# Optimization experiments

Hardware: AMD Instinct MI355X
Metric: run time of the kernel (lower is better)

Reference implementation:

```python
import jax, jax.numpy as jnp
import numpy as np

MAX_LENGTH = 13
PAD_TOKEN = 0
HIDDEN = 1024
VOCAB = 32000
BATCH = 64


def gru_cell(x, h, w_ih, w_hh, b_ih, b_hh):
    # PyTorch GRU gate order: reset, update, new
    gi = x @ w_ih.T + b_ih            # [B, 3H]
    gh = h @ w_hh.T + b_hh            # [B, 3H]
    i_r, i_z, i_n = jnp.split(gi, 3, axis=-1)
    h_r, h_z, h_n = jnp.split(gh, 3, axis=-1)
    r = jax.nn.sigmoid(i_r + h_r)
    z = jax.nn.sigmoid(i_z + h_z)
    n = jnp.tanh(i_n + r * h_n)
    return (1.0 - z) * n + z * h


def setup_inputs() -> dict:
    key = jax.random.key(0)
    ks = jax.random.split(key, 9)
    s = 0.02
    return {
        "encoder_outputs": jax.random.normal(ks[0], (BATCH, MAX_LENGTH, HIDDEN), jnp.float32),
        "encoder_hidden": jax.random.normal(ks[1], (1, BATCH, HIDDEN), jnp.float32),
        "embedding": jax.random.normal(ks[2], (VOCAB, HIDDEN), jnp.float32) * s,
        "w_ih": jax.random.normal(ks[3], (3 * HIDDEN, HIDDEN), jnp.float32) * s,
        "w_hh": jax.random.normal(ks[4], (3 * HIDDEN, HIDDEN), jnp.float32) * s,
        "b_ih": jnp.zeros((3 * HIDDEN,), jnp.float32),
        "b_hh": jnp.zeros((3 * HIDDEN,), jnp.float32),
        "w_out": jax.random.normal(ks[5], (VOCAB, HIDDEN), jnp.float32) * s,
        "b_out": jnp.zeros((VOCAB,), jnp.float32),
    }


def reference(encoder_outputs, encoder_hidden, embedding, w_ih, w_hh, b_ih, b_hh, w_out, b_out):
    batch = encoder_outputs.shape[0]
    h0 = encoder_hidden[0]                               # [B, H]
    tok0 = jnp.full((batch,), PAD_TOKEN, dtype=jnp.int32)

    def step(carry, _):
        h, tok = carry
        x = jax.nn.relu(embedding[tok])                  # embed + relu
        h = gru_cell(x, h, w_ih, w_hh, b_ih, b_hh)       # GRU cell
        logits = h @ w_out.T + b_out                     # [B, V]
        nxt = jnp.argmax(logits, axis=-1).astype(jnp.int32)  # greedy feedback (topk(1))
        return (h, nxt), logits

    (h_final, _), logits = jax.lax.scan(step, (h0, tok0), None, length=MAX_LENGTH)
    logits = jnp.transpose(logits, (1, 0, 2))            # [B, T, V]
    log_probs = jax.nn.log_softmax(logits, axis=-1)
    return log_probs, h_final[None]
```

## Files before the change

kernel.cpp:

```cpp
#include <hip/hip_runtime.h>
#include <math.h>

#define BB 64
#define HH 1024
#define VV 32000
#define TT 13
#define QS 8000
#define BKL 128

typedef float f32x4 __attribute__((ext_vector_type(4)));
typedef __bf16 bf16x8 __attribute__((ext_vector_type(8)));

__device__ __forceinline__ unsigned short f2bf(float f) {
  unsigned u = __float_as_uint(f);
  u = (u + 0x7fffu + ((u >> 16) & 1u)) >> 16;
  return (unsigned short)u;
}
__device__ __forceinline__ float bf2f(unsigned short s) {
  return __uint_as_float(((unsigned)s) << 16);
}

__device__ __forceinline__ void gld16(const void* g, void* l) {
  __builtin_amdgcn_global_load_lds(
      (const __attribute__((address_space(1))) unsigned int*)g,
      (__attribute__((address_space(3))) unsigned int*)l, 16, 0, 0);
}

__global__ __launch_bounds__(1024) void k_init(
    const float* __restrict__ enc, const float* __restrict__ emb,
    float* __restrict__ hrm, unsigned short* __restrict__ hhi,
    unsigned short* __restrict__ hlo, unsigned short* __restrict__ xhi,
    unsigned short* __restrict__ xlo) {
  const int g = blockIdx.x * 1024 + threadIdx.x;
  const float h = enc[g];
  hrm[g] = h;
  const unsigned short h16 = f2bf(h);
  hhi[g] = h16;
  hlo[g] = f2bf(h - bf2f(h16));
  float e = emb[threadIdx.x];
  e = e > 0.f ? e : 0.f;
  const unsigned short e16 = f2bf(e);
  xhi[g] = e16;
  xlo[g] = f2bf(e - bf2f(e16));
}

__global__ __launch_bounds__(256) void k_wconv(const float* __restrict__ w,
                                               unsigned short* __restrict__ o) {
  const int n4 = VV * HH / 4;
  for (int i = blockIdx.x * 256 + threadIdx.x; i < n4; i += gridDim.x * 256) {
    const f32x4 v = ((const f32x4*)w)[i];
    ushort4 u;
    u.x = f2bf(v[0]); u.y = f2bf(v[1]); u.z = f2bf(v[2]); u.w = f2bf(v[3]);
    ((ushort4*)o)[i] = u;
  }
}

__global__ __launch_bounds__(256) void k_wconv2(
    const float* __restrict__ wih, const float* __restrict__ whh,
    unsigned short* __restrict__ ghi, unsigned short* __restrict__ glo) {
  const int n4 = 6 * HH * HH / 4;
  for (int i = blockIdx.x * 256 + threadIdx.x; i < n4; i += gridDim.x * 256) {
    const int flat = i * 4;
    const float* src = flat < 3 * HH * HH ? wih + flat : whh + (flat - 3 * HH * HH);
    const f32x4 v = *(const f32x4*)src;
    ushort4 hi, lo;
    hi.x = f2bf(v[0]); lo.x = f2bf(v[0] - bf2f(hi.x));
    hi.y = f2bf(v[1]); lo.y = f2bf(v[1] - bf2f(hi.y));
    hi.z = f2bf(v[2]); lo.z = f2bf(v[2] - bf2f(hi.z));
    hi.w = f2bf(v[3]); lo.w = f2bf(v[3] - bf2f(hi.w));
    ((ushort4*)ghi)[i] = hi;
    ((ushort4*)glo)[i] = lo;
  }
}

__global__ __launch_bounds__(64) void k_gru(
    const unsigned short* __restrict__ xhi, const unsigned short* __restrict__ xlo,
    const unsigned short* __restrict__ hhi_s, const unsigned short* __restrict__ hlo_s,
    const unsigned short* __restrict__ ghi, const unsigned short* __restrict__ glo,
    const float* __restrict__ wih, const float* __restrict__ whh,
    float* __restrict__ gbuf, int cachegw) {
  const int blk = blockIdx.x, lane = threadIdx.x;
  const int kh = blk & 1;
  const int r2 = blk >> 1;
  const int g6 = r2 % 6, jt = r2 / 6;
  const unsigned short* Ahi = g6 < 3 ? xhi : hhi_s;
  const unsigned short* Alo = g6 < 3 ? xlo : hlo_s;
  const int cl = lane & 15, kk = (lane >> 4) * 8;
  const int j = jt * 16 + cl;
  const int kbeg = kh * 512;
  f32x4 acc[4];
  acc[0] = acc[1] = acc[2] = acc[3] = (f32x4){0.f, 0.f, 0.f, 0.f};

  if (cachegw) {
    const unsigned short* bh = ghi + (size_t)(g6 * HH + j) * HH + kbeg;
    const unsigned short* bl = glo + (size_t)(g6 * HH + j) * HH + kbeg;
    const unsigned short* ah = Ahi + kbeg;
    const unsigned short* al = Alo + kbeg;
    #pragma unroll 4
    for (int k0 = 0; k0 < 512; k0 += 32) {
      const bf16x8 whi = *(const bf16x8*)(bh + k0 + kk);
      const bf16x8 wlo = *(const bf16x8*)(bl + k0 + kk);
      #pragma unroll
      for (int rt = 0; rt < 4; ++rt) {
        const size_t aoff = (size_t)(rt * 16 + cl) * HH + k0 + kk;
        const bf16x8 a_h = *(const bf16x8*)(ah + aoff);
        const bf16x8 a_l = *(const bf16x8*)(al + aoff);
        acc[rt] = __builtin_amdgcn_mfma_f32_16x16x32_bf16(a_h, whi, acc[rt], 0, 0, 0);
        acc[rt] = __builtin_amdgcn_mfma_f32_16x16x32_bf16(a_l, whi, acc[rt], 0, 0, 0);
        acc[rt] = __builtin_amdgcn_mfma_f32_16x16x32_bf16(a_h, wlo, acc[rt], 0, 0, 0);
      }
    }
  } else {
    const float* W = (g6 < 3 ? wih : whh) + (size_t)((g6 % 3) * HH + j) * HH + kbeg;
    for (int k0 = 0; k0 < 512; k0 += 32) {
      const f32x4 w0 = *(const f32x4*)(W + k0 + kk);
      const f32x4 w1 = *(const f32x4*)(W + k0 + kk + 4);
      union { unsigned short u[8]; bf16x8 b; } chi, clo;
      #pragma unroll
      for (int u2 = 0; u2 < 4; ++u2) {
        chi.u[u2] = f2bf(w0[u2]); clo.u[u2] = f2bf(w0[u2] - bf2f(chi.u[u2]));
        chi.u[4 + u2] = f2bf(w1[u2]); clo.u[4 + u2] = f2bf(w1[u2] - bf2f(chi.u[4 + u2]));
      }
      #pragma unroll
      for (int rt = 0; rt < 4; ++rt) {
        const size_t aoff = (size_t)(rt * 16 + cl) * HH + kbeg + k0 + kk;
        const bf16x8 a_h = *(const bf16x8*)(Ahi + aoff);
        const bf16x8 a_l = *(const bf16x8*)(Alo + aoff);
        acc[rt] = __builtin_amdgcn_mfma_f32_16x16x32_bf16(a_h, chi.b, acc[rt], 0, 0, 0);
        acc[rt] = __builtin_amdgcn_mfma_f32_16x16x32_bf16(a_l, chi.b, acc[rt], 0, 0, 0);
        acc[rt] = __builtin_amdgcn_mfma_f32_16x16x32_bf16(a_h, clo.b, acc[rt], 0, 0, 0);
      }
    }
  }
  #pragma unroll
  for (int rt = 0; rt < 4; ++rt)
    #pragma unroll
    for (int rg = 0; rg < 4; ++rg) {
      const int row = rt * 16 + (lane >> 4) * 4 + rg;
      gbuf[(size_t)((kh * 6 + g6) * BB + row) * HH + jt * 16 + cl] = acc[rt][rg];
    }
}

__global__ __launch_bounds__(256) void k_gep(
    const float* __restrict__ gbuf, const float* __restrict__ bih,
    const float* __restrict__ bhh, const float* __restrict__ hsrc,
    float* __restrict__ hdst, unsigned short* __restrict__ hhi_d,
    unsigned short* __restrict__ hlo_d) {
  const int e = blockIdx.x * 256 + threadIdx.x;
  const int b = e >> 10, j = e & (HH - 1);
  const size_t base = (size_t)b * HH + j;
  const float gir = gbuf[(size_t)(0 * BB + b) * HH + j] + gbuf[(size_t)((6 + 0) * BB + b) * HH + j] + bih[j];
  const float giz = gbuf[(size_t)(1 * BB + b) * HH + j] + gbuf[(size_t)((6 + 1) * BB + b) * HH + j] + bih[HH + j];
  const float gin = gbuf[(size_t)(2 * BB + b) * HH + j] + gbuf[(size_t)((6 + 2) * BB + b) * HH + j] + bih[2 * HH + j];
  const float ghr = gbuf[(size_t)(3 * BB + b) * HH + j] + gbuf[(size_t)((6 + 3) * BB + b) * HH + j] + bhh[j];
  const float ghz = gbuf[(size_t)(4 * BB + b) * HH + j] + gbuf[(size_t)((6 + 4) * BB + b) * HH + j] + bhh[HH + j];
  const float ghn = gbuf[(size_t)(5 * BB + b) * HH + j] + gbuf[(size_t)((6 + 5) * BB + b) * HH + j] + bhh[2 * HH + j];
  const float r_ = 1.f / (1.f + __expf(-(gir + ghr)));
  const float z_ = 1.f / (1.f + __expf(-(giz + ghz)));
  const float n_ = tanhf(gin + r_ * ghn);
  const float hnew = (1.f - z_) * n_ + z_ * hsrc[base];
  hdst[base] = hnew;
  const unsigned short h16 = f2bf(hnew);
  hhi_d[base] = h16;
  hlo_d[base] = f2bf(hnew - bf2f(h16));
}

__global__ __launch_bounds__(512, 1) void k_logits_lds(
    const unsigned short* __restrict__ hb,
    const unsigned short* __restrict__ wbf,
    const float* __restrict__ bout, float* __restrict__ lbuf) {
  __shared__ __attribute__((aligned(16))) unsigned char sA[2][64 * BKL * 2];
  __shared__ __attribute__((aligned(16))) unsigned char sB[2][128 * BKL * 2];
  const int tid = threadIdx.x, blk = blockIdx.x;
  const int lane = tid & 63, wv = tid >> 6;
  const int cl = lane & 15, kk = (lane >> 4) * 8;

  auto STAGE = [&](int buf, int k0) {
    #pragma unroll
    for (int it = 0; it < 2; ++it) {
      const int c = it * 512 + tid;
      const int r = c >> 4;
      const int kb = (c & 15) * 16;
      const int kbs = kb ^ ((r & 7) << 4);
      gld16(hb + (size_t)r * HH + k0 + (kbs >> 1),
            &sA[buf][it * 8192 + wv * 1024]);
    }
    #pragma unroll
    for (int it = 0; it < 4; ++it) {
      const int c = it * 512 + tid;
      const int col = c >> 4;
      const int kb = (c & 15) * 16;
      const int kbs = kb ^ ((col & 7) << 4);
      gld16(wbf + (size_t)(blk * 128 + col) * HH + k0 + (kbs >> 1),
            &sB[buf][it * 8192 + wv * 1024]);
    }
  };

  f32x4 acc[4];
  acc[0] = acc[1] = acc[2] = acc[3] = (f32x4){0.f, 0.f, 0.f, 0.f};

  STAGE(0, 0);
  for (int t = 0; t < HH / BKL; ++t) {
    const int cur = t & 1;
    if (t < HH / BKL - 1) {
      STAGE(cur ^ 1, (t + 1) * BKL);
      asm volatile("s_waitcnt vmcnt(6)" ::: "memory");
    } else {
      asm volatile("s_waitcnt vmcnt(0)" ::: "memory");
    }
    __builtin_amdgcn_s_barrier();
    __builtin_amdgcn_sched_barrier(0);
    #pragma unroll
    for (int ks = 0; ks < BKL; ks += 32) {
      const int bc = wv * 16 + cl;
      const bf16x8 bfr = *(const bf16x8*)&sB[cur][bc * (BKL * 2) + (((ks + kk) * 2) ^ ((bc & 7) << 4))];
      #pragma unroll
      for (int rt = 0; rt < 4; ++rt) {
        const int ar = rt * 16 + cl;
        const bf16x8 afr = *(const bf16x8*)&sA[cur][ar * (BKL * 2) + (((ks + kk) * 2) ^ ((ar & 7) << 4))];
        acc[rt] = __builtin_amdgcn_mfma_f32_16x16x32_bf16(afr, bfr, acc[rt], 0, 0, 0);
      }
    }
    __builtin_amdgcn_s_barrier();
    __builtin_amdgcn_sched_barrier(0);
  }

  const int col = blk * 128 + wv * 16 + cl;
  const float bo = bout[col];
  #pragma unroll
  for (int rt = 0; rt < 4; ++rt)
    #pragma unroll
    for (int rg = 0; rg < 4; ++rg) {
      const int row = rt * 16 + (lane >> 4) * 4 + rg;
      lbuf[(size_t)row * VV + col] = acc[rt][rg] + bo;
    }
}

__global__ __launch_bounds__(256) void k_logits_fb(
    const unsigned short* __restrict__ hb, const float* __restrict__ wout,
    const float* __restrict__ bout, float* __restrict__ lbuf) {
  const int tid = threadIdx.x, blk = blockIdx.x;
  const int lane = tid & 63, wv = tid >> 6;
  const int n0 = blk * 64 + wv * 16;
  const int cl = lane & 15, kk = (lane >> 4) * 8;
  f32x4 acc[4];
  acc[0] = acc[1] = acc[2] = acc[3] = (f32x4){0.f, 0.f, 0.f, 0.f};
  const float* wrow = wout + (size_t)(n0 + cl) * HH;
  for (int k0 = 0; k0 < HH; k0 += 32) {
    const f32x4 w0 = *(const f32x4*)(wrow + k0 + kk);
    const f32x4 w1 = *(const f32x4*)(wrow + k0 + kk + 4);
    union { unsigned short u[8]; bf16x8 b; } cv;
    #pragma unroll
    for (int u2 = 0; u2 < 4; ++u2) { cv.u[u2] = f2bf(w0[u2]); cv.u[4 + u2] = f2bf(w1[u2]); }
    #pragma unroll
    for (int rt = 0; rt < 4; ++rt) {
      const bf16x8 afr = *(const bf16x8*)(hb + (size_t)(rt * 16 + cl) * HH + k0 + kk);
      acc[rt] = __builtin_amdgcn_mfma_f32_16x16x32_bf16(afr, cv.b, acc[rt], 0, 0, 0);
    }
  }
  const int col = n0 + cl;
  const float bo = bout[col];
  #pragma unroll
  for (int rt = 0; rt < 4; ++rt)
    #pragma unroll
    for (int rg = 0; rg < 4; ++rg) {
      const int row = rt * 16 + (lane >> 4) * 4 + rg;
      lbuf[(size_t)row * VV + col] = acc[rt][rg] + bo;
    }
}

__global__ __launch_bounds__(256) void k_sum(
    const float* __restrict__ lbuf, const float* __restrict__ wout,
    const float* __restrict__ bout, const float* __restrict__ hnew,
    float* __restrict__ mq, float* __restrict__ sq,
    float* __restrict__ qbestV, int* __restrict__ qbestI, int dorecheck) {
  __shared__ float srow[QS];
  __shared__ float red[4];
  __shared__ int icnt;
  __shared__ int scand[32];
  const int tid = threadIdx.x;
  const int b = blockIdx.x >> 2, q = blockIdx.x & 3;
  const int lane = tid & 63, wv = tid >> 6;
  const f32x4* src = (const f32x4*)(lbuf + (size_t)b * VV + q * QS);
  f32x4* s4 = (f32x4*)srow;

  float m = -3.0e38f;
  for (int i = tid; i < QS / 4; i += 256) {
    const f32x4 v = src[i];
    s4[i] = v;
    m = fmaxf(fmaxf(fmaxf(m, v[0]), v[1]), fmaxf(v[2], v[3]));
  }
  #pragma unroll
  for (int d = 1; d < 64; d <<= 1) m = fmaxf(m, __shfl_xor(m, d, 64));
  if (lane == 0) red[wv] = m;
  if (tid == 0) icnt = 0;
  __syncthreads();
  const float M = fmaxf(fmaxf(red[0], red[1]), fmaxf(red[2], red[3]));

  float s = 0.f;
  for (int i = tid; i < QS / 4; i += 256) {
    const f32x4 v = s4[i];
    s += __expf(v[0] - M) + __expf(v[1] - M) + __expf(v[2] - M) + __expf(v[3] - M);
  }
  #pragma unroll
  for (int d = 1; d < 64; d <<= 1) s += __shfl_xor(s, d, 64);
  __syncthreads();
  if (lane == 0) red[wv] = s;
  __syncthreads();
  if (tid == 0) {
    mq[b * 4 + q] = M;
    sq[b * 4 + q] = red[0] + red[1] + red[2] + red[3];
  }

  if (dorecheck) {
    const float thr = M - 0.05f;
    for (int i = tid; i < QS / 4; i += 256) {
      const f32x4 v = s4[i];
      #pragma unroll
      for (int u = 0; u < 4; ++u)
        if (v[u] >= thr) {
          const int c = atomicAdd(&icnt, 1);
          if (c < 32) scand[c] = q * QS + 4 * i + u;
        }
    }
    __syncthreads();
    if (wv == 0) {
      const int nc = icnt < 32 ? icnt : 32;
      const float* hrow = hnew + (size_t)b * HH;
      f32x4 h4[4];
      #pragma unroll
      for (int u = 0; u < 4; ++u) h4[u] = *(const f32x4*)(hrow + lane * 16 + u * 4);
      float best = -3.0e38f; int bi = 0x7fffffff;
      for (int ci = 0; ci < nc; ++ci) {
        const int v = scand[ci];
        const float* wrow = wout + (size_t)v * HH + lane * 16;
        float ss = 0.f;
        #pragma unroll
        for (int u = 0; u < 4; ++u) {
          const f32x4 w4 = *(const f32x4*)(wrow + u * 4);
          ss += h4[u][0] * w4[0] + h4[u][1] * w4[1] + h4[u][2] * w4[2] + h4[u][3] * w4[3];
        }
        #pragma unroll
        for (int d = 1; d < 64; d <<= 1) ss += __shfl_xor(ss, d, 64);
        ss += bout[v];
        if (ss > best || (ss == best && v < bi)) { best = ss; bi = v; }
      }
      if (lane == 0) { qbestV[b * 4 + q] = best; qbestI[b * 4 + q] = bi; }
    }
  }
}

__global__ __launch_bounds__(256) void k_out(
    const float* __restrict__ lbuf, const float* __restrict__ mq,
    const float* __restrict__ sq, const float* __restrict__ qbestV,
    const int* __restrict__ qbestI, const float* __restrict__ emb,
    const float* __restrict__ hnew, float* __restrict__ out,
    unsigned short* __restrict__ xhi, unsigned short* __restrict__ xlo, int t) {
  __shared__ int stok;
  const int tid = threadIdx.x;
  const int b = blockIdx.x >> 2, q = blockIdx.x & 3;

  const float m0 = mq[b * 4 + 0], m1 = mq[b * 4 + 1];
  const float m2 = mq[b * 4 + 2], m3 = mq[b * 4 + 3];
  const float Mg = fmaxf(fmaxf(m0, m1), fmaxf(m2, m3));
  const float Sg = sq[b * 4 + 0] * __expf(m0 - Mg) + sq[b * 4 + 1] * __expf(m1 - Mg) +
                   sq[b * 4 + 2] * __expf(m2 - Mg) + sq[b * 4 + 3] * __expf(m3 - Mg);
  const float LZ = Mg + logf(Sg);

  const f32x4* src = (const f32x4*)(lbuf + (size_t)b * VV + q * QS);
  f32x4* dst = (f32x4*)(out + ((size_t)b * TT + t) * VV + q * QS);
  for (int i = tid; i < QS / 4; i += 256)
    dst[i] = src[i] - LZ;

  if (q == 0 && t < TT - 1) {
    if (tid == 0) {
      float bv = qbestV[b * 4 + 0]; int bi = qbestI[b * 4 + 0];
      #pragma unroll
      for (int qq = 1; qq < 4; ++qq) {
        const float v = qbestV[b * 4 + qq]; const int i2 = qbestI[b * 4 + qq];
        if (v > bv || (v == bv && i2 < bi)) { bv = v; bi = i2; }
      }
      stok = bi;
    }
    __syncthreads();
    const int tok = stok;
    for (int j = tid; j < HH; j += 256) {
      float e = emb[(size_t)tok * HH + j];
      e = e > 0.f ? e : 0.f;
      const unsigned short e16 = f2bf(e);
      xhi[(size_t)b * HH + j] = e16;
      xlo[(size_t)b * HH + j] = f2bf(e - bf2f(e16));
    }
  }
  if (q == 0 && t == TT - 1) {
    for (int j = tid; j < HH; j += 256)
      out[(size_t)BB * TT * VV + (size_t)b * HH + j] = hnew[(size_t)b * HH + j];
  }
}

extern "C" void kernel_launch(void* const* d_in, const int* in_sizes, int n_in,
                              void* d_out, int out_size, void* d_ws, size_t ws_size,
                              hipStream_t stream) {
  const float* enc  = (const float*)d_in[1];
  const float* emb  = (const float*)d_in[2];
  const float* wih  = (const float*)d_in[3];
  const float* whh  = (const float*)d_in[4];
  const float* bih  = (const float*)d_in[5];
  const float* bhh  = (const float*)d_in[6];
  const float* wout = (const float*)d_in[7];
  const float* bout = (const float*)d_in[8];
  float* out = (float*)d_out;

  char* ws = (char*)d_ws;
  size_t off = 0;
  auto alloc = [&](size_t bytes) -> char* {
    char* p = ws + off;
    off += (bytes + 255) & ~(size_t)255;
    return p;
  };
  float* hrm = (float*)alloc((size_t)2 * BB * HH * 4);
  unsigned short* hhi = (unsigned short*)alloc((size_t)2 * BB * HH * 2);
  unsigned short* hlo = (unsigned short*)alloc((size_t)2 * BB * HH * 2);
  unsigned short* xhi = (unsigned short*)alloc((size_t)BB * HH * 2);
  unsigned short* xlo = (unsigned short*)alloc((size_t)BB * HH * 2);
  float* gbuf = (float*)alloc((size_t)12 * BB * HH * 4);
  float* lbuf = (float*)alloc((size_t)BB * VV * 4);
  float* mq = (float*)alloc((size_t)BB * 4 * 4);
  float* sq = (float*)alloc((size_t)BB * 4 * 4);
  float* qbestV = (float*)alloc((size_t)BB * 4 * 4);
  int* qbestI = (int*)alloc((size_t)BB * 4 * 4);
  unsigned short* wbf = (unsigned short*)alloc((size_t)VV * HH * 2);
  const int cachew = (ws_size >= off) ? 1 : 0;
  unsigned short* ghi = (unsigned short*)alloc((size_t)6 * HH * HH * 2);
  unsigned short* glo = (unsigned short*)alloc((size_t)6 * HH * HH * 2);
  const int cachegw = (ws_size >= off) ? 1 : 0;

  hipLaunchKernelGGL(k_init, dim3(64), dim3(1024), 0, stream,
                     enc, emb, hrm, hhi, hlo, xhi, xlo);
  if (cachew)
    hipLaunchKernelGGL(k_wconv, dim3(2048), dim3(256), 0, stream, wout, wbf);
  if (cachegw)
    hipLaunchKernelGGL(k_wconv2, dim3(1024), dim3(256), 0, stream, wih, whh, ghi, glo);

  for (int t = 0; t < TT; ++t) {
    const int p = t & 1;
    const float* hsrc = hrm + (size_t)p * BB * HH;
    float* hdst = hrm + (size_t)(p ^ 1) * BB * HH;
    const unsigned short* hhs = hhi + (size_t)p * BB * HH;
    const unsigned short* hls = hlo + (size_t)p * BB * HH;
    unsigned short* hhd = hhi + (size_t)(p ^ 1) * BB * HH;
    unsigned short* hld = hlo + (size_t)(p ^ 1) * BB * HH;

    hipLaunchKernelGGL(k_gru, dim3(768), dim3(64), 0, stream,
                       xhi, xlo, hhs, hls, ghi, glo, wih, whh, gbuf, cachegw);
    hipLaunchKernelGGL(k_gep, dim3(256), dim3(256), 0, stream,
                       gbuf, bih, bhh, hsrc, hdst, hhd, hld);
    if (cachew)
      hipLaunchKernelGGL(k_logits_lds, dim3(250), dim3(512), 0, stream,
                         hhd, wbf, bout, lbuf);
    else
      hipLaunchKernelGGL(k_logits_fb, dim3(500), dim3(256), 0, stream,
                         hhd, wout, bout, lbuf);
    hipLaunchKernelGGL(k_sum, dim3(256), dim3(256), 0, stream,
                       lbuf, wout, bout, hdst, mq, sq, qbestV, qbestI,
                       (t < TT - 1) ? 1 : 0);
    hipLaunchKernelGGL(k_out, dim3(256), dim3(256), 0, stream,
                       lbuf, mq, sq, qbestV, qbestI, emb, hdst, out, xhi, xlo, t);
  }
}
```

Baseline: 927.0 us.

## Fuse GRU gate GEMM and elementwise epilogue into one kernel via LDS

Merges the GRU gate matmul and the gate epilogue into a single kernel. Each of 64 blocks of 12 waves computes all six gate slices and both K-halves for 16 hidden columns, reduces them through shared memory, and writes the new hidden state directly. This removes the global gbuf round trip and one kernel launch per timestep. The trade-off is only 64 workgroups instead of 768, which may underuse the GPU's many CUs during the GEMM phase.

```diff
diff --git a/kernel.cpp b/kernel.cpp
--- a/kernel.cpp
+++ b/kernel.cpp
@@ -73,29 +73,29 @@
   }
 }
 
-__global__ __launch_bounds__(64) void k_gru(
+__global__ __launch_bounds__(768, 1) void k_gruF(
     const unsigned short* __restrict__ xhi, const unsigned short* __restrict__ xlo,
     const unsigned short* __restrict__ hhi_s, const unsigned short* __restrict__ hlo_s,
     const unsigned short* __restrict__ ghi, const unsigned short* __restrict__ glo,
-    const float* __restrict__ wih, const float* __restrict__ whh,
-    float* __restrict__ gbuf, int cachegw) {
-  const int blk = blockIdx.x, lane = threadIdx.x;
-  const int kh = blk & 1;
-  const int r2 = blk >> 1;
-  const int g6 = r2 % 6, jt = r2 / 6;
-  const unsigned short* Ahi = g6 < 3 ? xhi : hhi_s;
-  const unsigned short* Alo = g6 < 3 ? xlo : hlo_s;
+    const float* __restrict__ bih, const float* __restrict__ bhh,
+    const float* __restrict__ hsrc, float* __restrict__ hdst,
+    unsigned short* __restrict__ hhi_d, unsigned short* __restrict__ hlo_d) {
+  __shared__ float g[12][64][17];
+  const int blk = blockIdx.x, tid = threadIdx.x;
+  const int lane = tid & 63, wv = tid >> 6;
+  const int g6 = wv % 6, kh = wv / 6;
   const int cl = lane & 15, kk = (lane >> 4) * 8;
-  const int j = jt * 16 + cl;
+  const int j = blk * 16 + cl;
   const int kbeg = kh * 512;
-  f32x4 acc[4];
-  acc[0] = acc[1] = acc[2] = acc[3] = (f32x4){0.f, 0.f, 0.f, 0.f};
-
-  if (cachegw) {
+  {
+    const unsigned short* Ahi = g6 < 3 ? xhi : hhi_s;
+    const unsigned short* Alo = g6 < 3 ? xlo : hlo_s;
     const unsigned short* bh = ghi + (size_t)(g6 * HH + j) * HH + kbeg;
     const unsigned short* bl = glo + (size_t)(g6 * HH + j) * HH + kbeg;
     const unsigned short* ah = Ahi + kbeg;
     const unsigned short* al = Alo + kbeg;
+    f32x4 acc[4];
+    acc[0] = acc[1] = acc[2] = acc[3] = (f32x4){0.f, 0.f, 0.f, 0.f};
     #pragma unroll 4
     for (int k0 = 0; k0 < 512; k0 += 32) {
       const bf16x8 whi = *(const bf16x8*)(bh + k0 + kk);
@@ -110,59 +110,32 @@
         acc[rt] = __builtin_amdgcn_mfma_f32_16x16x32_bf16(a_h, wlo, acc[rt], 0, 0, 0);
       }
     }
-  } else {
-    const float* W = (g6 < 3 ? wih : whh) + (size_t)((g6 % 3) * HH + j) * HH + kbeg;
-    for (int k0 = 0; k0 < 512; k0 += 32) {
-      const f32x4 w0 = *(const f32x4*)(W + k0 + kk);
-      const f32x4 w1 = *(const f32x4*)(W + k0 + kk + 4);
-      union { unsigned short u[8]; bf16x8 b; } chi, clo;
+    #pragma unroll
+    for (int rt = 0; rt < 4; ++rt)
       #pragma unroll
-      for (int u2 = 0; u2 < 4; ++u2) {
-        chi.u[u2] = f2bf(w0[u2]); clo.u[u2] = f2bf(w0[u2] - bf2f(chi.u[u2]));
-        chi.u[4 + u2] = f2bf(w1[u2]); clo.u[4 + u2] = f2bf(w1[u2] - bf2f(chi.u[4 + u2]));
-      }
-      #pragma unroll
-      for (int rt = 0; rt < 4; ++rt) {
-        const size_t aoff = (size_t)(rt * 16 + cl) * HH + kbeg + k0 + kk;
-        const bf16x8 a_h = *(const bf16x8*)(Ahi + aoff);
-        const bf16x8 a_l = *(const bf16x8*)(Alo + aoff);
-        acc[rt] = __builtin_amdgcn_mfma_f32_16x16x32_bf16(a_h, chi.b, acc[rt], 0, 0, 0);
-        acc[rt] = __builtin_amdgcn_mfma_f32_16x16x32_bf16(a_l, chi.b, acc[rt], 0, 0, 0);
-        acc[rt] = __builtin_amdgcn_mfma_f32_16x16x32_bf16(a_h, clo.b, acc[rt], 0, 0, 0);
-      }
-    }
-  }
-  #pragma unroll
-  for (int rt = 0; rt < 4; ++rt)
-    #pragma unroll
-    for (int rg = 0; rg < 4; ++rg) {
-      const int row = rt * 16 + (lane >> 4) * 4 + rg;
-      gbuf[(size_t)((kh * 6 + g6) * BB + row) * HH + jt * 16 + cl] = acc[rt][rg];
-    }
-}
-
-__global__ __launch_bounds__(256) void k_gep(
-    const float* __restrict__ gbuf, const float* __restrict__ bih,
-    const float* __restrict__ bhh, const float* __restrict__ hsrc,
-    float* __restrict__ hdst, unsigned short* __restrict__ hhi_d,
-    unsigned short* __restrict__ hlo_d) {
-  const int e = blockIdx.x * 256 + threadIdx.x;
-  const int b = e >> 10, j = e & (HH - 1);
-  const size_t base = (size_t)b * HH + j;
-  const float gir = gbuf[(size_t)(0 * BB + b) * HH + j] + gbuf[(size_t)((6 + 0) * BB + b) * HH + j] + bih[j];
-  const float giz = gbuf[(size_t)(1 * BB + b) * HH + j] + gbuf[(size_t)((6 + 1) * BB + b) * HH + j] + bih[HH + j];
-  const float gin = gbuf[(size_t)(2 * BB + b) * HH + j] + gbuf[(size_t)((6 + 2) * BB + b) * HH + j] + bih[2 * HH + j];
-  const float ghr = gbuf[(size_t)(3 * BB + b) * HH + j] + gbuf[(size_t)((6 + 3) * BB + b) * HH + j] + bhh[j];
-  const float ghz = gbuf[(size_t)(4 * BB + b) * HH + j] + gbuf[(size_t)((6 + 4) * BB + b) * HH + j] + bhh[HH + j];
-  const float ghn = gbuf[(size_t)(5 * BB + b) * HH + j] + gbuf[(size_t)((6 + 5) * BB + b) * HH + j] + bhh[2 * HH + j];
-  const float r_ = 1.f / (1.f + __expf(-(gir + ghr)));
-  const float z_ = 1.f / (1.f + __expf(-(giz + ghz)));
-  const float n_ = tanhf(gin + r_ * ghn);
-  const float hnew = (1.f - z_) * n_ + z_ * hsrc[base];
-  hdst[base] = hnew;
-  const unsigned short h16 = f2bf(hnew);
-  hhi_d[base] = h16;
-  hlo_d[base] = f2bf(hnew - bf2f(h16));
+      for (int rg = 0; rg < 4; ++rg)
+        g[wv][rt * 16 + (lane >> 4) * 4 + rg][cl] = acc[rt][rg];
+  }
+  __syncthreads();
+  for (int e = tid; e < BB * 16; e += 768) {
+    const int b = e >> 4, c = e & 15;
+    const int jj = blk * 16 + c;
+    const size_t base = (size_t)b * HH + jj;
+    const float gir = g[0][b][c] + g[6][b][c] + bih[jj];
+    const float giz = g[1][b][c] + g[7][b][c] + bih[HH + jj];
+    const float gin = g[2][b][c] + g[8][b][c] + bih[2 * HH + jj];
+    const float ghr = g[3][b][c] + g[9][b][c] + bhh[jj];
+    const float ghz = g[4][b][c] + g[10][b][c] + bhh[HH + jj];
+    const float ghn = g[5][b][c] + g[11][b][c] + bhh[2 * HH + jj];
+    const float r_ = 1.f / (1.f + __expf(-(gir + ghr)));
+    const float z_ = 1.f / (1.f + __expf(-(giz + ghz)));
+    const float n_ = tanhf(gin + r_ * ghn);
+    const float hnew = (1.f - z_) * n_ + z_ * hsrc[base];
+    hdst[base] = hnew;
+    const unsigned short h16 = f2bf(hnew);
+    hhi_d[base] = h16;
+    hlo_d[base] = f2bf(hnew - bf2f(h16));
+  }
 }
 
 __global__ __launch_bounds__(512, 1) void k_logits_lds(
@@ -226,39 +199,6 @@
   }
 
   const int col = blk * 128 + wv * 16 + cl;
-  const float bo = bout[col];
-  #pragma unroll
-  for (int rt = 0; rt < 4; ++rt)
-    #pragma unroll
-    for (int rg = 0; rg < 4; ++rg) {
-      const int row = rt * 16 + (lane >> 4) * 4 + rg;
-      lbuf[(size_t)row * VV + col] = acc[rt][rg] + bo;
-    }
-}
-
-__global__ __launch_bounds__(256) void k_logits_fb(
-    const unsigned short* __restrict__ hb, const float* __restrict__ wout,
-    const float* __restrict__ bout, float* __restrict__ lbuf) {
-  const int tid = threadIdx.x, blk = blockIdx.x;
-  const int lane = tid & 63, wv = tid >> 6;
-  const int n0 = blk * 64 + wv * 16;
-  const int cl = lane & 15, kk = (lane >> 4) * 8;
-  f32x4 acc[4];
-  acc[0] = acc[1] = acc[2] = acc[3] = (f32x4){0.f, 0.f, 0.f, 0.f};
-  const float* wrow = wout + (size_t)(n0 + cl) * HH;
-  for (int k0 = 0; k0 < HH; k0 += 32) {
-    const f32x4 w0 = *(const f32x4*)(wrow + k0 + kk);
-    const f32x4 w1 = *(const f32x4*)(wrow + k0 + kk + 4);
-    union { unsigned short u[8]; bf16x8 b; } cv;
-    #pragma unroll
-    for (int u2 = 0; u2 < 4; ++u2) { cv.u[u2] = f2bf(w0[u2]); cv.u[4 + u2] = f2bf(w1[u2]); }
-    #pragma unroll
-    for (int rt = 0; rt < 4; ++rt) {
-      const bf16x8 afr = *(const bf16x8*)(hb + (size_t)(rt * 16 + cl) * HH + k0 + kk);
-      acc[rt] = __builtin_amdgcn_mfma_f32_16x16x32_bf16(afr, cv.b, acc[rt], 0, 0, 0);
-    }
-  }
-  const int col = n0 + cl;
   const float bo = bout[col];
   #pragma unroll
   for (int rt = 0; rt < 4; ++rt)
@@ -398,6 +338,108 @@
   }
 }
 
+__global__ __launch_bounds__(64) void k_gru_fb(
+    const unsigned short* __restrict__ xhi, const unsigned short* __restrict__ xlo,
+    const unsigned short* __restrict__ hhi_s, const unsigned short* __restrict__ hlo_s,
+    const float* __restrict__ wih, const float* __restrict__ whh,
+    float* __restrict__ gbuf) {
+  const int blk = blockIdx.x, lane = threadIdx.x;
+  const int kh = blk & 1;
+  const int r2 = blk >> 1;
+  const int g6 = r2 % 6, jt = r2 / 6;
+  const unsigned short* Ahi = g6 < 3 ? xhi : hhi_s;
+  const unsigned short* Alo = g6 < 3 ? xlo : hlo_s;
+  const int cl = lane & 15, kk = (lane >> 4) * 8;
+  const int j = jt * 16 + cl;
+  const int kbeg = kh * 512;
+  f32x4 acc[4];
+  acc[0] = acc[1] = acc[2] = acc[3] = (f32x4){0.f, 0.f, 0.f, 0.f};
+  const float* W = (g6 < 3 ? wih : whh) + (size_t)((g6 % 3) * HH + j) * HH + kbeg;
+  for (int k0 = 0; k0 < 512; k0 += 32) {
+    const f32x4 w0 = *(const f32x4*)(W + k0 + kk);
+    const f32x4 w1 = *(const f32x4*)(W + k0 + kk + 4);
+    union { unsigned short u[8]; bf16x8 b; } chi, clo;
+    #pragma unroll
+    for (int u2 = 0; u2 < 4; ++u2) {
+      chi.u[u2] = f2bf(w0[u2]); clo.u[u2] = f2bf(w0[u2] - bf2f(chi.u[u2]));
+      chi.u[4 + u2] = f2bf(w1[u2]); clo.u[4 + u2] = f2bf(w1[u2] - bf2f(chi.u[4 + u2]));
+    }
+    #pragma unroll
+    for (int rt = 0; rt < 4; ++rt) {
+      const size_t aoff = (size_t)(rt * 16 + cl) * HH + kbeg + k0 + kk;
+      const bf16x8 a_h = *(const bf16x8*)(Ahi + aoff);
+      const bf16x8 a_l = *(const bf16x8*)(Alo + aoff);
+      acc[rt] = __builtin_amdgcn_mfma_f32_16x16x32_bf16(a_h, chi.b, acc[rt], 0, 0, 0);
+      acc[rt] = __builtin_amdgcn_mfma_f32_16x16x32_bf16(a_l, chi.b, acc[rt], 0, 0, 0);
+      acc[rt] = __builtin_amdgcn_mfma_f32_16x16x32_bf16(a_h, clo.b, acc[rt], 0, 0, 0);
+    }
+  }
+  #pragma unroll
+  for (int rt = 0; rt < 4; ++rt)
+    #pragma unroll
+    for (int rg = 0; rg < 4; ++rg) {
+      const int row = rt * 16 + (lane >> 4) * 4 + rg;
+      gbuf[(size_t)((kh * 6 + g6) * BB + row) * HH + jt * 16 + cl] = acc[rt][rg];
+    }
+}
+
+__global__ __launch_bounds__(256) void k_gep(
+    const float* __restrict__ gbuf, const float* __restrict__ bih,
+    const float* __restrict__ bhh, const float* __restrict__ hsrc,
+    float* __restrict__ hdst, unsigned short* __restrict__ hhi_d,
+    unsigned short* __restrict__ hlo_d) {
+  const int e = blockIdx.x * 256 + threadIdx.x;
+  const int b = e >> 10, j = e & (HH - 1);
+  const size_t base = (size_t)b * HH + j;
+  const float gir = gbuf[(size_t)(0 * BB + b) * HH + j] + gbuf[(size_t)((6 + 0) * BB + b) * HH + j] + bih[j];
+  const float giz = gbuf[(size_t)(1 * BB + b) * HH + j] + gbuf[(size_t)((6 + 1) * BB + b) * HH + j] + bih[HH + j];
+  const float gin = gbuf[(size_t)(2 * BB + b) * HH + j] + gbuf[(size_t)((6 + 2) * BB + b) * HH + j] + bih[2 * HH + j];
+  const float ghr = gbuf[(size_t)(3 * BB + b) * HH + j] + gbuf[(size_t)((6 + 3) * BB + b) * HH + j] + bhh[j];
+  const float ghz = gbuf[(size_t)(4 * BB + b) * HH + j] + gbuf[(size_t)((6 + 4) * BB + b) * HH + j] + bhh[HH + j];
+  const float ghn = gbuf[(size_t)(5 * BB + b) * HH + j] + gbuf[(size_t)((6 + 5) * BB + b) * HH + j] + bhh[2 * HH + j];
+  const float r_ = 1.f / (1.f + __expf(-(gir + ghr)));
+  const float z_ = 1.f / (1.f + __expf(-(giz + ghz)));
+  const float n_ = tanhf(gin + r_ * ghn);
+  const float hnew = (1.f - z_) * n_ + z_ * hsrc[base];
+  hdst[base] = hnew;
+  const unsigned short h16 = f2bf(hnew);
+  hhi_d[base] = h16;
+  hlo_d[base] = f2bf(hnew - bf2f(h16));
+}
+
+__global__ __launch_bounds__(256) void k_logits_fb(
+    const unsigned short* __restrict__ hb, const float* __restrict__ wout,
+    const float* __restrict__ bout, float* __restrict__ lbuf) {
+  const int tid = threadIdx.x, blk = blockIdx.x;
+  const int lane = tid & 63, wv = tid >> 6;
+  const int n0 = blk * 64 + wv * 16;
+  const int cl = lane & 15, kk = (lane >> 4) * 8;
+  f32x4 acc[4];
+  acc[0] = acc[1] = acc[2] = acc[3] = (f32x4){0.f, 0.f, 0.f, 0.f};
+  const float* wrow = wout + (size_t)(n0 + cl) * HH;
+  for (int k0 = 0; k0 < HH; k0 += 32) {
+    const f32x4 w0 = *(const f32x4*)(wrow + k0 + kk);
+    const f32x4 w1 = *(const f32x4*)(wrow + k0 + kk + 4);
+    union { unsigned short u[8]; bf16x8 b; } cv;
+    #pragma unroll
+    for (int u2 = 0; u2 < 4; ++u2) { cv.u[u2] = f2bf(w0[u2]); cv.u[4 + u2] = f2bf(w1[u2]); }
+    #pragma unroll
+    for (int rt = 0; rt < 4; ++rt) {
+      const bf16x8 afr = *(const bf16x8*)(hb + (size_t)(rt * 16 + cl) * HH + k0 + kk);
+      acc[rt] = __builtin_amdgcn_mfma_f32_16x16x32_bf16(afr, cv.b, acc[rt], 0, 0, 0);
+    }
+  }
+  const int col = n0 + cl;
+  const float bo = bout[col];
+  #pragma unroll
+  for (int rt = 0; rt < 4; ++rt)
+    #pragma unroll
+    for (int rg = 0; rg < 4; ++rg) {
+      const int row = rt * 16 + (lane >> 4) * 4 + rg;
+      lbuf[(size_t)row * VV + col] = acc[rt][rg] + bo;
+    }
+}
+
 extern "C" void kernel_launch(void* const* d_in, const int* in_sizes, int n_in,
                               void* d_out, int out_size, void* d_ws, size_t ws_size,
                               hipStream_t stream) {
@@ -430,17 +472,16 @@
   float* qbestV = (float*)alloc((size_t)BB * 4 * 4);
   int* qbestI = (int*)alloc((size_t)BB * 4 * 4);
   unsigned short* wbf = (unsigned short*)alloc((size_t)VV * HH * 2);
-  const int cachew = (ws_size >= off) ? 1 : 0;
   unsigned short* ghi = (unsigned short*)alloc((size_t)6 * HH * HH * 2);
   unsigned short* glo = (unsigned short*)alloc((size_t)6 * HH * HH * 2);
-  const int cachegw = (ws_size >= off) ? 1 : 0;
+  const int cache_ok = (ws_size >= off) ? 1 : 0;
 
   hipLaunchKernelGGL(k_init, dim3(64), dim3(1024), 0, stream,
                      enc, emb, hrm, hhi, hlo, xhi, xlo);
-  if (cachew)
+  if (cache_ok) {
     hipLaunchKernelGGL(k_wconv, dim3(2048), dim3(256), 0, stream, wout, wbf);
-  if (cachegw)
     hipLaunchKernelGGL(k_wconv2, dim3(1024), dim3(256), 0, stream, wih, whh, ghi, glo);
+  }
 
   for (int t = 0; t < TT; ++t) {
     const int p = t & 1;
@@ -451,16 +492,20 @@
     unsigned short* hhd = hhi + (size_t)(p ^ 1) * BB * HH;
     unsigned short* hld = hlo + (size_t)(p ^ 1) * BB * HH;
 
-    hipLaunchKernelGGL(k_gru, dim3(768), dim3(64), 0, stream,
-                       xhi, xlo, hhs, hls, ghi, glo, wih, whh, gbuf, cachegw);
-    hipLaunchKernelGGL(k_gep, dim3(256), dim3(256), 0, stream,
-                       gbuf, bih, bhh, hsrc, hdst, hhd, hld);
-    if (cachew)
+    if (cache_ok) {
+      hipLaunchKernelGGL(k_gruF, dim3(64), dim3(768), 0, stream,
+                         xhi, xlo, hhs, hls, ghi, glo, bih, bhh,
+                         hsrc, hdst, hhd, hld);
       hipLaunchKernelGGL(k_logits_lds, dim3(250), dim3(512), 0, stream,
                          hhd, wbf, bout, lbuf);
-    else
+    } else {
+      hipLaunchKernelGGL(k_gru_fb, dim3(768), dim3(64), 0, stream,
+                         xhi, xlo, hhs, hls, wih, whh, gbuf);
+      hipLaunchKernelGGL(k_gep, dim3(256), dim3(256), 0, stream,
+                         gbuf, bih, bhh, hsrc, hdst, hhd, hld);
       hipLaunchKernelGGL(k_logits_fb, dim3(500), dim3(256), 0, stream,
                          hhd, wout, bout, lbuf);
+    }
     hipLaunchKernelGGL(k_sum, dim3(256), dim3(256), 0, stream,
                        lbuf, wout, bout, hdst, mq, sq, qbestV, qbestI,
                        (t < TT - 1) ? 1 : 0);
```

Measured after the change: 1.395 ms. 50.5% more time.
